# Performance work log

Hardware: AMD Instinct MI355X
Metric: run time of the kernel (lower is better)

Reference implementation:

```python
import jax, jax.numpy as jnp
import numpy as np


def setup_inputs() -> dict:
    key = jax.random.key(0)
    ks = jax.random.split(key, 4)
    B, M, D = 512, 40, 64
    # split_half=True with layers [200,200,200]: prev = 40 -> 100 -> 100
    x = jax.random.normal(ks[0], (B, M, D), dtype=jnp.float32)
    w1 = jax.random.normal(ks[1], (200, M * 40), dtype=jnp.float32) * 0.02
    w2 = jax.random.normal(ks[2], (200, M * 100), dtype=jnp.float32) * 0.02
    w3 = jax.random.normal(ks[3], (200, M * 100), dtype=jnp.float32) * 0.02
    b1 = jnp.zeros((200,), dtype=jnp.float32)
    b2 = jnp.zeros((200,), dtype=jnp.float32)
    b3 = jnp.zeros((200,), dtype=jnp.float32)
    return {"x": x, "w1": w1, "b1": b1, "w2": w2, "b2": b2, "w3": w3, "b3": b3}


def reference(x, w1, b1, w2, b2, w3, b3):
    B, M, D = x.shape
    params = [(w1, b1), (w2, b2), (w3, b3)]
    n_layers = len(params)
    hidden = x  # (B, prev, D), starts as x0
    outs = []
    for i, (w, b) in enumerate(params):
        # outer product over field dims, flattened channel-major as in torch .view
        outer = jnp.einsum('bmd,bnd->bmnd', x, hidden).reshape(B, -1, D)
        # Conv1d kernel_size=1 == per-position linear over channels
        out = jax.nn.relu(jnp.einsum('bcd,oc->bod', outer, w) + b[None, :, None])
        if i < n_layers - 1:  # split_half
            half = out.shape[1] // 2
            out, direct = out[:, :half, :], out[:, half:, :]
            outs.append(direct)
        else:
            outs.append(out)
        hidden = out
    return jnp.concatenate(outs, axis=1).sum(axis=2)  # (B, 100+100+200)
```

## Files before the change

### kernel.cpp

```cpp
#include <hip/hip_runtime.h>
#include <hip/hip_bf16.h>


typedef float f32x4 __attribute__((ext_vector_type(4)));
typedef short bf16x8 __attribute__((ext_vector_type(8)));
typedef unsigned int uint;

#define XS_STR 44
#define HS_STR 108

struct LDSState {
    __hip_bfloat16 xs[2][64][XS_STR];
    __hip_bfloat16 hs[2][2][64][HS_STR];
    uint U[8][2][64][16];
};

static __device__ __forceinline__ float bflo(uint u) {
    uint v = u << 16; return __builtin_bit_cast(float, v);
}
static __device__ __forceinline__ float bfhi(uint u) {
    uint v = u & 0xffff0000u; return __builtin_bit_cast(float, v);
}
static __device__ __forceinline__ uint pk_bf16(float a, float b) {
    uint r; asm("v_cvt_pk_bf16_f32 %0, %1, %2" : "=v"(r) : "v"(a), "v"(b));
    return r;
}

#define PHASE_BAR() do {                                   \
    asm volatile("s_waitcnt lgkmcnt(0)" ::: "memory");     \
    __builtin_amdgcn_sched_barrier(0);                     \
    __builtin_amdgcn_s_barrier();                          \
    __builtin_amdgcn_sched_barrier(0);                     \
} while (0)

template<int DIV, int NK, int HASH, int ROWLO, int ROWOFF, int HSTR, int A>
__device__ __forceinline__ void layer_core(
    LDSState* L, const bf16x8* __restrict__ wpk, const float* __restrict__ bias,
    const __hip_bfloat16* __restrict__ h0, const __hip_bfloat16* __restrict__ h1,
    int dstpp, float* outb0, float* outb1, int tid, int mt0)
{
    const int lane = tid & 63;
    const int wv = tid >> 6, wn = wv & 1;
    const int q = lane >> 4, lr = lane & 15, d = lane;

    const int hdr = (lr >> 1) & 7;
    const uint* ub  = &L->U[0][0][0][0] + wn * 1024;
    const uint* roA = ub + (lr * 16 + 2 * ((2 * q) ^ hdr));
    const uint* roB = ub + (lr * 16 + 2 * ((2 * q + 1) ^ hdr));

    const int hdw = (d >> 1) & 7;
    uint* wb = &L->U[0][0][d][0] + 2 * (wv ^ hdw);

    const __hip_bfloat16* xb0 = &L->xs[0][d][0];
    const __hip_bfloat16* xb1 = &L->xs[1][d][0];
    const __hip_bfloat16* hb0 = h0 + d * HSTR;
    const __hip_bfloat16* hb1 = h1 + d * HSTR;

    f32x4 acc[A][4];
    #pragma unroll
    for (int mi = 0; mi < A; ++mi)
        #pragma unroll
        for (int nj = 0; nj < 4; ++nj)
            acc[mi][nj] = {0.f, 0.f, 0.f, 0.f};

    int bm = (4 * wv) / DIV;
    int bn = (4 * wv) % DIV;
    int bk = 0;
    auto build = [&]() {
        if (bk < NK) {
            const int slab_dw = (bk & 7) * 2048;
            float xf0 = __bfloat162float(xb0[bm]);
            float xf1 = __bfloat162float(xb1[bm]);
            uint2 ha = *(const uint2*)(hb0 + bn);
            uint2 hc = *(const uint2*)(hb1 + bn);
            uint2 w0, w1;
            w0.x = pk_bf16(xf0 * bflo(ha.x), xf0 * bfhi(ha.x));
            w0.y = pk_bf16(xf0 * bflo(ha.y), xf0 * bfhi(ha.y));
            w1.x = pk_bf16(xf1 * bflo(hc.x), xf1 * bfhi(hc.x));
            w1.y = pk_bf16(xf1 * bflo(hc.y), xf1 * bfhi(hc.y));
            *(uint2*)(wb + slab_dw)        = w0;
            *(uint2*)(wb + slab_dw + 1024) = w1;
            bn += 32;
            if (bn >= DIV) { bn -= DIV; ++bm; }
            ++bk;
        }
    };

    auto consume = [&](int slab_dw, bf16x8* f) {
        bf16x8 bv[4];
        #pragma unroll
        for (int nj = 0; nj < 4; ++nj) {
            union { uint2 u2[2]; bf16x8 v; } t;
            t.u2[0] = *(const uint2*)(roA + slab_dw + nj * 256);
            t.u2[1] = *(const uint2*)(roB + slab_dw + nj * 256);
            bv[nj] = t.v;
        }
        #pragma unroll
        for (int mi = 0; mi < A; ++mi)
            #pragma unroll
            for (int nj = 0; nj < 4; ++nj)
                acc[mi][nj] = __builtin_amdgcn_mfma_f32_16x16x32_bf16(
                    f[mi], bv[nj], acc[mi][nj], 0, 0, 0);
    };

    const bf16x8* pw = wpk + (size_t)mt0 * NK * 64 + lane;
    auto loadf = [&](bf16x8* f, int s) {
        if (s < NK) {
            #pragma unroll
            for (int mi = 0; mi < A; ++mi)
                f[mi] = pw[(size_t)mi * NK * 64 + (size_t)s * 64];
        }
    };

    bf16x8 a0[A], a1[A], a2[A], a3[A], b0[A], b1[A], b2[A], b3[A];
    loadf(a0, 0); loadf(a1, 1); loadf(a2, 2); loadf(a3, 3);
    loadf(b0, 4); loadf(b1, 5); loadf(b2, 6); loadf(b3, 7);
    build(); build(); build(); build();
    __syncthreads();

    #pragma unroll 1
    for (int s = 0; s + 8 <= NK; s += 8) {
        consume(0 * 2048, a0); loadf(a0, s + 8);
        consume(1 * 2048, a1); loadf(a1, s + 9);
        consume(2 * 2048, a2); loadf(a2, s + 10);
        consume(3 * 2048, a3); loadf(a3, s + 11);
        build(); build(); build(); build();
        PHASE_BAR();
        consume(4 * 2048, b0); loadf(b0, s + 12);
        consume(5 * 2048, b1); loadf(b1, s + 13);
        consume(6 * 2048, b2); loadf(b2, s + 14);
        consume(7 * 2048, b3); loadf(b3, s + 15);
        build(); build(); build(); build();
        PHASE_BAR();
    }
    constexpr int REM = NK % 8;
    if constexpr (REM >= 1) consume(0 * 2048, a0);
    if constexpr (REM >= 2) consume(1 * 2048, a1);
    if constexpr (REM >= 3) consume(2 * 2048, a2);
    if constexpr (REM >= 4) consume(3 * 2048, a3);
    if constexpr (REM == 5) {
        build();
        PHASE_BAR();
        consume(4 * 2048, b0);
    }

    float* outp = wn ? outb1 : outb0;
    #pragma unroll
    for (int mi = 0; mi < A; ++mi) {
        const int mt = mt0 + mi;
        #pragma unroll
        for (int reg = 0; reg < 4; ++reg) {
            const int o = 16 * mt + 4 * q + reg;
            if (o < 200) {
                const float bs = bias[o];
                float r0 = fmaxf(acc[mi][0][reg] + bs, 0.f);
                float r1 = fmaxf(acc[mi][1][reg] + bs, 0.f);
                float r2 = fmaxf(acc[mi][2][reg] + bs, 0.f);
                float r3 = fmaxf(acc[mi][3][reg] + bs, 0.f);
                if (HASH && o < 100) {
                    L->hs[dstpp][wn][ 0 + lr][o] = __float2bfloat16(r0);
                    L->hs[dstpp][wn][16 + lr][o] = __float2bfloat16(r1);
                    L->hs[dstpp][wn][32 + lr][o] = __float2bfloat16(r2);
                    L->hs[dstpp][wn][48 + lr][o] = __float2bfloat16(r3);
                }
                if (o >= ROWLO) {
                    float sv = (r0 + r1) + (r2 + r3);
                    sv += __shfl_xor(sv, 1, 64);
                    sv += __shfl_xor(sv, 2, 64);
                    sv += __shfl_xor(sv, 4, 64);
                    sv += __shfl_xor(sv, 8, 64);
                    if (lr == 0) outp[ROWOFF + (o - ROWLO)] = sv;
                }
            }
        }
    }
    __syncthreads();
}

template<int A>
__device__ __forceinline__ void run_layers(
    LDSState* L, const bf16x8* w1p, const bf16x8* w2p, const bf16x8* w3p,
    const float* b1, const float* b2, const float* b3,
    float* outb0, float* outb1, int tid, int mt0)
{
    layer_core< 40,  50, 1, 100,   0, XS_STR, A>(L, w1p, b1,
        &L->xs[0][0][0], &L->xs[1][0][0], 0, outb0, outb1, tid, mt0);
    layer_core<100, 125, 1, 100, 100, HS_STR, A>(L, w2p, b2,
        &L->hs[0][0][0][0], &L->hs[0][1][0][0], 1, outb0, outb1, tid, mt0);
    layer_core<100, 125, 0,   0, 200, HS_STR, A>(L, w3p, b3,
        &L->hs[1][0][0][0], &L->hs[1][1][0][0], 0, outb0, outb1, tid, mt0);
}

__global__ __launch_bounds__(512, 2)
void fused_mfma(const float* __restrict__ x,
                const bf16x8* __restrict__ wpk,
                const float* __restrict__ b1, const float* __restrict__ b2,
                const float* __restrict__ b3, float* __restrict__ out) {
    __shared__ LDSState L;
    const int tid = threadIdx.x;
    const int bi  = blockIdx.x;

    const float* xg = x + (size_t)(2 * bi) * 2560;
    for (int i = tid; i < 5120; i += 512) {
        int bb = (i >= 2560) ? 1 : 0;
        int r  = i - bb * 2560;
        L.xs[bb][r & 63][r >> 6] = __float2bfloat16(xg[(size_t)bb * 2560 + r]);
    }
    __syncthreads();

    float* outb0 = out + (size_t)(2 * bi + 0) * 400;
    float* outb1 = out + (size_t)(2 * bi + 1) * 400;

    const bf16x8* w1p = wpk;
    const bf16x8* w2p = wpk + 41600;
    const bf16x8* w3p = wpk + 145600;

    const int wm = tid >> 7;
    if (wm == 0)
        run_layers<4>(&L, w1p, w2p, w3p, b1, b2, b3, outb0, outb1, tid, 0);
    else
        run_layers<3>(&L, w1p, w2p, w3p, b1, b2, b3, outb0, outb1, tid,
                      3 * wm + 1);
}

__global__ void convert_pack(const float* __restrict__ w1, const float* __restrict__ w2,
                             const float* __restrict__ w3, uint4* __restrict__ outp) {
    int c = blockIdx.x * 256 + threadIdx.x;
    if (c >= 249600) return;
    const float* src; int K, base;
    if (c < 41600)       { src = w1; K = 1600; base = c; }
    else if (c < 145600) { src = w2; K = 4000; base = c - 41600; }
    else                 { src = w3; K = 4000; base = c - 145600; }
    const int NS   = K / 32;
    const int lane = base & 63;
    const int t    = base >> 6;
    const int mt   = t / NS;
    const int s    = t - mt * NS;
    const int row  = 16 * mt + (lane & 15);
    const int k0   = 32 * s + 8 * (lane >> 4);
    uint o[4];
    if (row < 200) {
        const float* p = src + (size_t)row * K + k0;
        #pragma unroll
        for (int j = 0; j < 4; ++j) {
            __hip_bfloat16 lo = __float2bfloat16(p[2 * j]);
            __hip_bfloat16 hi = __float2bfloat16(p[2 * j + 1]);
            o[j] = (uint)__builtin_bit_cast(unsigned short, lo)
                 | ((uint)__builtin_bit_cast(unsigned short, hi) << 16);
        }
    } else {
        #pragma unroll
        for (int j = 0; j < 4; ++j) o[j] = 0u;
    }
    uint4 v; v.x = o[0]; v.y = o[1]; v.z = o[2]; v.w = o[3];
    outp[c] = v;
}

__global__ __launch_bounds__(512, 1)
void fused_bilinear_kernel(const float* __restrict__ x,
                           const float* __restrict__ w1, const float* __restrict__ b1,
                           const float* __restrict__ w2, const float* __restrict__ b2,
                           const float* __restrict__ w3, const float* __restrict__ b3,
                           float* __restrict__ out) {
    const int b   = blockIdx.x;
    const int tid = threadIdx.x;
    const int d   = tid & 63;
    const int wv  = tid >> 6;

    __shared__ float xs[40][64];
    __shared__ float hs[100][64];

    const float* xb = x + (size_t)b * 40 * 64;
    for (int i = tid; i < 40 * 64; i += 512) ((float*)xs)[i] = xb[i];
    __syncthreads();

    float xr[40];
    #pragma unroll
    for (int m = 0; m < 40; ++m) xr[m] = xs[m][d];
    float hr[100];
    const int o0 = __builtin_amdgcn_readfirstlane(wv * 25);

    for (int oi = 0; oi < 25; ++oi) {
        const int o = o0 + oi;
        const float* __restrict__ wrow = w1 + (size_t)o * 1600;
        float s = b1[o];
        for (int m = 0; m < 40; ++m) {
            const float* __restrict__ wm = wrow + m * 40;
            float a0 = 0.f, a1 = 0.f, a2 = 0.f, a3 = 0.f;
            #pragma unroll
            for (int n = 0; n < 40; n += 4) {
                a0 = fmaf(wm[n + 0], xr[n + 0], a0);
                a1 = fmaf(wm[n + 1], xr[n + 1], a1);
                a2 = fmaf(wm[n + 2], xr[n + 2], a2);
                a3 = fmaf(wm[n + 3], xr[n + 3], a3);
            }
            s = fmaf(xs[m][d], (a0 + a1) + (a2 + a3), s);
        }
        s = fmaxf(s, 0.f);
        if (o < 100) hs[o][d] = s;
        else {
            float r = s;
            #pragma unroll
            for (int off = 32; off > 0; off >>= 1) r += __shfl_xor(r, off, 64);
            if (d == 0) out[(size_t)b * 400 + (o - 100)] = r;
        }
    }
    __syncthreads();
    #pragma unroll
    for (int n = 0; n < 100; ++n) hr[n] = hs[n][d];
    __syncthreads();

    for (int oi = 0; oi < 25; ++oi) {
        const int o = o0 + oi;
        const float* __restrict__ wrow = w2 + (size_t)o * 4000;
        float s = b2[o];
        for (int m = 0; m < 40; ++m) {
            const float* __restrict__ wm = wrow + m * 100;
            float a0 = 0.f, a1 = 0.f, a2 = 0.f, a3 = 0.f;
            #pragma unroll
            for (int n = 0; n < 100; n += 4) {
                a0 = fmaf(wm[n + 0], hr[n + 0], a0);
                a1 = fmaf(wm[n + 1], hr[n + 1], a1);
                a2 = fmaf(wm[n + 2], hr[n + 2], a2);
                a3 = fmaf(wm[n + 3], hr[n + 3], a3);
            }
            s = fmaf(xs[m][d], (a0 + a1) + (a2 + a3), s);
        }
        s = fmaxf(s, 0.f);
        if (o < 100) hs[o][d] = s;
        else {
            float r = s;
            #pragma unroll
            for (int off = 32; off > 0; off >>= 1) r += __shfl_xor(r, off, 64);
            if (d == 0) out[(size_t)b * 400 + 100 + (o - 100)] = r;
        }
    }
    __syncthreads();
    #pragma unroll
    for (int n = 0; n < 100; ++n) hr[n] = hs[n][d];

    for (int oi = 0; oi < 25; ++oi) {
        const int o = o0 + oi;
        const float* __restrict__ wrow = w3 + (size_t)o * 4000;
        float s = b3[o];
        for (int m = 0; m < 40; ++m) {
            const float* __restrict__ wm = wrow + m * 100;
            float a0 = 0.f, a1 = 0.f, a2 = 0.f, a3 = 0.f;
            #pragma unroll
            for (int n = 0; n < 100; n += 4) {
                a0 = fmaf(wm[n + 0], hr[n + 0], a0);
                a1 = fmaf(wm[n + 1], hr[n + 1], a1);
                a2 = fmaf(wm[n + 2], hr[n + 2], a2);
                a3 = fmaf(wm[n + 3], hr[n + 3], a3);
            }
            s = fmaf(xs[m][d], (a0 + a1) + (a2 + a3), s);
        }
        s = fmaxf(s, 0.f);
        float r = s;
        #pragma unroll
        for (int off = 32; off > 0; off >>= 1) r += __shfl_xor(r, off, 64);
        if (d == 0) out[(size_t)b * 400 + 200 + o] = r;
    }
}

extern "C" void kernel_launch(void* const* d_in, const int* in_sizes, int n_in,
                              void* d_out, int out_size, void* d_ws, size_t ws_size,
                              hipStream_t stream) {
    const float* x  = (const float*)d_in[0];
    const float* w1 = (const float*)d_in[1];
    const float* b1 = (const float*)d_in[2];
    const float* w2 = (const float*)d_in[3];
    const float* b2 = (const float*)d_in[4];
    const float* w3 = (const float*)d_in[5];
    const float* b3 = (const float*)d_in[6];
    float* out = (float*)d_out;

    if (ws_size >= 249600u * 16u) {
        uint4* wp = (uint4*)d_ws;
        convert_pack<<<dim3(975), dim3(256), 0, stream>>>(w1, w2, w3, wp);
        fused_mfma<<<dim3(256), dim3(512), 0, stream>>>(
            x, (const bf16x8*)wp, b1, b2, b3, out);
    } else {
        fused_bilinear_kernel<<<dim3(512), dim3(512), 0, stream>>>(
            x, w1, b1, w2, b2, w3, b3, out);
    }
}
```

Baseline: 158.7 us.

## Specialize waves into producer builders and MFMA consumers

Splits the 8 waves of each block into 6 consumer waves that only run MFMA over 13 output tiles (5/4/4 per pair) and 2 producer waves that only build the bf16 outer-product operand slabs in LDS. Previously every wave both built and consumed. The weight-register prefetch depth drops from 8 to 4 slabs, and the build/consume phases alternate across half-slab-rings separated by barriers. This removes the build ALU work from the MFMA waves. In exchange, fewer waves issue MFMAs, each consumer wave holds more accumulators, and producer throughput may become the bottleneck.

```diff
diff --git a/kernel.cpp b/kernel.cpp
--- a/kernel.cpp
+++ b/kernel.cpp
@@ -33,7 +33,7 @@
     __builtin_amdgcn_sched_barrier(0);                     \
 } while (0)
 
-template<int DIV, int NK, int HASH, int ROWLO, int ROWOFF, int HSTR, int A>
+template<int DIV, int NK, int HASH, int ROWLO, int ROWOFF, int HSTR, int A, int CONS>
 __device__ __forceinline__ void layer_core(
     LDSState* L, const bf16x8* __restrict__ wpk, const float* __restrict__ bias,
     const __hip_bfloat16* __restrict__ h0, const __hip_bfloat16* __restrict__ h1,
@@ -49,7 +49,8 @@
     const uint* roB = ub + (lr * 16 + 2 * ((2 * q + 1) ^ hdr));
 
     const int hdw = (d >> 1) & 7;
-    uint* wb = &L->U[0][0][d][0] + 2 * (wv ^ hdw);
+    uint* wbp = &L->U[0][0][d][0];
+    const int pp = wv & 1;
 
     const __hip_bfloat16* xb0 = &L->xs[0][d][0];
     const __hip_bfloat16* xb1 = &L->xs[1][d][0];
@@ -57,31 +58,41 @@
     const __hip_bfloat16* hb1 = h1 + d * HSTR;
 
     f32x4 acc[A][4];
+    if constexpr (CONS) {
+        #pragma unroll
+        for (int mi = 0; mi < A; ++mi)
+            #pragma unroll
+            for (int nj = 0; nj < 4; ++nj)
+                acc[mi][nj] = {0.f, 0.f, 0.f, 0.f};
+    }
+
+    int pm[4], pn[4];
     #pragma unroll
-    for (int mi = 0; mi < A; ++mi)
-        #pragma unroll
-        for (int nj = 0; nj < 4; ++nj)
-            acc[mi][nj] = {0.f, 0.f, 0.f, 0.f};
-
-    int bm = (4 * wv) / DIV;
-    int bn = (4 * wv) % DIV;
+    for (int g = 0; g < 4; ++g) {
+        const int c0 = 16 * pp + 4 * g;
+        pm[g] = c0 / DIV; pn[g] = c0 % DIV;
+    }
     int bk = 0;
     auto build = [&]() {
         if (bk < NK) {
             const int slab_dw = (bk & 7) * 2048;
-            float xf0 = __bfloat162float(xb0[bm]);
-            float xf1 = __bfloat162float(xb1[bm]);
-            uint2 ha = *(const uint2*)(hb0 + bn);
-            uint2 hc = *(const uint2*)(hb1 + bn);
-            uint2 w0, w1;
-            w0.x = pk_bf16(xf0 * bflo(ha.x), xf0 * bfhi(ha.x));
-            w0.y = pk_bf16(xf0 * bflo(ha.y), xf0 * bfhi(ha.y));
-            w1.x = pk_bf16(xf1 * bflo(hc.x), xf1 * bfhi(hc.x));
-            w1.y = pk_bf16(xf1 * bflo(hc.y), xf1 * bfhi(hc.y));
-            *(uint2*)(wb + slab_dw)        = w0;
-            *(uint2*)(wb + slab_dw + 1024) = w1;
-            bn += 32;
-            if (bn >= DIV) { bn -= DIV; ++bm; }
+            #pragma unroll
+            for (int g = 0; g < 4; ++g) {
+                float xf0 = __bfloat162float(xb0[pm[g]]);
+                float xf1 = __bfloat162float(xb1[pm[g]]);
+                uint2 ha = *(const uint2*)(hb0 + pn[g]);
+                uint2 hc = *(const uint2*)(hb1 + pn[g]);
+                uint2 w0, w1;
+                w0.x = pk_bf16(xf0 * bflo(ha.x), xf0 * bfhi(ha.x));
+                w0.y = pk_bf16(xf0 * bflo(ha.y), xf0 * bfhi(ha.y));
+                w1.x = pk_bf16(xf1 * bflo(hc.x), xf1 * bfhi(hc.x));
+                w1.y = pk_bf16(xf1 * bflo(hc.y), xf1 * bfhi(hc.y));
+                const int pos = 2 * ((4 * pp + g) ^ hdw);
+                *(uint2*)(wbp + slab_dw + pos)        = w0;
+                *(uint2*)(wbp + slab_dw + 1024 + pos) = w1;
+                pn[g] += 32;
+                if (pn[g] >= DIV) { pn[g] -= DIV; ++pm[g]; }
+            }
             ++bk;
         }
     };
@@ -112,64 +123,80 @@
         }
     };
 
-    bf16x8 a0[A], a1[A], a2[A], a3[A], b0[A], b1[A], b2[A], b3[A];
-    loadf(a0, 0); loadf(a1, 1); loadf(a2, 2); loadf(a3, 3);
-    loadf(b0, 4); loadf(b1, 5); loadf(b2, 6); loadf(b3, 7);
-    build(); build(); build(); build();
+    bf16x8 a0[A], a1[A], a2[A], a3[A];
+    if constexpr (CONS) {
+        loadf(a0, 0); loadf(a1, 1); loadf(a2, 2); loadf(a3, 3);
+    } else {
+        build(); build(); build(); build();
+    }
     __syncthreads();
 
     #pragma unroll 1
     for (int s = 0; s + 8 <= NK; s += 8) {
-        consume(0 * 2048, a0); loadf(a0, s + 8);
-        consume(1 * 2048, a1); loadf(a1, s + 9);
-        consume(2 * 2048, a2); loadf(a2, s + 10);
-        consume(3 * 2048, a3); loadf(a3, s + 11);
-        build(); build(); build(); build();
+        if constexpr (CONS) {
+            consume(0,    a0); loadf(a0, s + 4);
+            consume(2048, a1); loadf(a1, s + 5);
+            consume(4096, a2); loadf(a2, s + 6);
+            consume(6144, a3); loadf(a3, s + 7);
+        } else {
+            build(); build(); build(); build();
+        }
         PHASE_BAR();
-        consume(4 * 2048, b0); loadf(b0, s + 12);
-        consume(5 * 2048, b1); loadf(b1, s + 13);
-        consume(6 * 2048, b2); loadf(b2, s + 14);
-        consume(7 * 2048, b3); loadf(b3, s + 15);
-        build(); build(); build(); build();
+        if constexpr (CONS) {
+            consume(8192,  a0); loadf(a0, s + 8);
+            consume(10240, a1); loadf(a1, s + 9);
+            consume(12288, a2); loadf(a2, s + 10);
+            consume(14336, a3); loadf(a3, s + 11);
+        } else {
+            build(); build(); build(); build();
+        }
         PHASE_BAR();
     }
     constexpr int REM = NK % 8;
-    if constexpr (REM >= 1) consume(0 * 2048, a0);
-    if constexpr (REM >= 2) consume(1 * 2048, a1);
-    if constexpr (REM >= 3) consume(2 * 2048, a2);
-    if constexpr (REM >= 4) consume(3 * 2048, a3);
-    if constexpr (REM == 5) {
-        build();
+    if constexpr (REM == 2) {
+        if constexpr (CONS) { consume(0, a0); consume(2048, a1); }
+    } else if constexpr (REM == 5) {
+        if constexpr (CONS) {
+            consume(0, a0);
+            loadf(a0, NK - 1);
+            consume(2048, a1);
+            consume(4096, a2);
+            consume(6144, a3);
+        } else {
+            build();
+        }
         PHASE_BAR();
-        consume(4 * 2048, b0);
-    }
-
-    float* outp = wn ? outb1 : outb0;
-    #pragma unroll
-    for (int mi = 0; mi < A; ++mi) {
-        const int mt = mt0 + mi;
-        #pragma unroll
-        for (int reg = 0; reg < 4; ++reg) {
-            const int o = 16 * mt + 4 * q + reg;
-            if (o < 200) {
-                const float bs = bias[o];
-                float r0 = fmaxf(acc[mi][0][reg] + bs, 0.f);
-                float r1 = fmaxf(acc[mi][1][reg] + bs, 0.f);
-                float r2 = fmaxf(acc[mi][2][reg] + bs, 0.f);
-                float r3 = fmaxf(acc[mi][3][reg] + bs, 0.f);
-                if (HASH && o < 100) {
-                    L->hs[dstpp][wn][ 0 + lr][o] = __float2bfloat16(r0);
-                    L->hs[dstpp][wn][16 + lr][o] = __float2bfloat16(r1);
-                    L->hs[dstpp][wn][32 + lr][o] = __float2bfloat16(r2);
-                    L->hs[dstpp][wn][48 + lr][o] = __float2bfloat16(r3);
-                }
-                if (o >= ROWLO) {
-                    float sv = (r0 + r1) + (r2 + r3);
-                    sv += __shfl_xor(sv, 1, 64);
-                    sv += __shfl_xor(sv, 2, 64);
-                    sv += __shfl_xor(sv, 4, 64);
-                    sv += __shfl_xor(sv, 8, 64);
-                    if (lr == 0) outp[ROWOFF + (o - ROWLO)] = sv;
+        if constexpr (CONS) consume(8192, a0);
+    }
+
+    if constexpr (CONS) {
+        float* outp = wn ? outb1 : outb0;
+        #pragma unroll
+        for (int mi = 0; mi < A; ++mi) {
+            const int mt = mt0 + mi;
+            #pragma unroll
+            for (int reg = 0; reg < 4; ++reg) {
+                const int o = 16 * mt + 4 * q + reg;
+                if (o < 200) {
+                    const float bs = bias[o];
+                    float r0 = fmaxf(acc[mi][0][reg] + bs, 0.f);
+                    float r1 = fmaxf(acc[mi][1][reg] + bs, 0.f);
+                    float r2 = fmaxf(acc[mi][2][reg] + bs, 0.f);
+                    float r3 = fmaxf(acc[mi][3][reg] + bs, 0.f);
+                    if (HASH && o < 100) {
+                        L->hs[dstpp][wn][ 0 + lr][o] = __float2bfloat16(r0);
+                        L->hs[dstpp][wn][16 + lr][o] = __float2bfloat16(r1);
+                        L->hs[dstpp][wn][32 + lr][o] = __float2bfloat16(r2);
+                        L->hs[dstpp][wn][48 + lr][o] = __float2bfloat16(r3);
+                    }
+                    if (o >= ROWLO) {
+                        float sv = (r0 + r1) + (r2 + r3);
+                        sv += __shfl_xor(sv, 1, 64);
+                        sv += __shfl_xor(sv, 2, 64);
+                        sv += __shfl_xor(sv, 4, 64);
+                        sv += __shfl_xor(sv, 8, 64);
+                        if (lr == 0) outp[ROWOFF + (o - ROWLO)] = sv;
+                    }
                 }
             }
         }
@@ -177,17 +204,17 @@
     __syncthreads();
 }
 
-template<int A>
+template<int A, int CONS>
 __device__ __forceinline__ void run_layers(
     LDSState* L, const bf16x8* w1p, const bf16x8* w2p, const bf16x8* w3p,
     const float* b1, const float* b2, const float* b3,
     float* outb0, float* outb1, int tid, int mt0)
 {
-    layer_core< 40,  50, 1, 100,   0, XS_STR, A>(L, w1p, b1,
+    layer_core< 40,  50, 1, 100,   0, XS_STR, A, CONS>(L, w1p, b1,
         &L->xs[0][0][0], &L->xs[1][0][0], 0, outb0, outb1, tid, mt0);
-    layer_core<100, 125, 1, 100, 100, HS_STR, A>(L, w2p, b2,
+    layer_core<100, 125, 1, 100, 100, HS_STR, A, CONS>(L, w2p, b2,
         &L->hs[0][0][0][0], &L->hs[0][1][0][0], 1, outb0, outb1, tid, mt0);
-    layer_core<100, 125, 0,   0, 200, HS_STR, A>(L, w3p, b3,
+    layer_core<100, 125, 0,   0, 200, HS_STR, A, CONS>(L, w3p, b3,
         &L->hs[1][0][0][0], &L->hs[1][1][0][0], 0, outb0, outb1, tid, mt0);
 }
 
@@ -215,12 +242,18 @@
     const bf16x8* w2p = wpk + 41600;
     const bf16x8* w3p = wpk + 145600;
 
-    const int wm = tid >> 7;
-    if (wm == 0)
-        run_layers<4>(&L, w1p, w2p, w3p, b1, b2, b3, outb0, outb1, tid, 0);
-    else
-        run_layers<3>(&L, w1p, w2p, w3p, b1, b2, b3, outb0, outb1, tid,
-                      3 * wm + 1);
+    const int wv = tid >> 6;
+    if (wv < 6) {
+        const int cm = wv >> 1;
+        if (cm == 0)
+            run_layers<5, 1>(&L, w1p, w2p, w3p, b1, b2, b3, outb0, outb1, tid, 0);
+        else if (cm == 1)
+            run_layers<4, 1>(&L, w1p, w2p, w3p, b1, b2, b3, outb0, outb1, tid, 5);
+        else
+            run_layers<4, 1>(&L, w1p, w2p, w3p, b1, b2, b3, outb0, outb1, tid, 9);
+    } else {
+        run_layers<1, 0>(&L, w1p, w2p, w3p, b1, b2, b3, outb0, outb1, tid, 0);
+    }
 }
 
 __global__ void convert_pack(const float* __restrict__ w1, const float* __restrict__ w2,
```

Result: slower. 208.2 us (+31.2%).
